# Kernel optimization log

Measured on AMD Instinct MI355X. Metric: run time of the kernel, lower is better.

## Reference

```python
import jax, jax.numpy as jnp
import numpy as np

D = 768       # feature dim (LayerNorm([768]))
NCHAR = 96    # codebook rows (char_dic = zeros(96, 768))
EPS = 1e-5    # torch LayerNorm default eps
EMA = 0.1     # EMA update coefficient


def layer_norm(x, w, b):
    mu = jnp.mean(x, axis=-1, keepdims=True)
    var = jnp.mean((x - mu) ** 2, axis=-1, keepdims=True)
    return (x - mu) * jax.lax.rsqrt(var + EPS) * w + b


def setup_inputs() -> dict:
    key = jax.random.key(0)
    k1, k2, k3 = jax.random.split(key, 3)
    B, S = 128, 1024
    return {
        "input_f": jax.random.normal(k1, (B, S, D), dtype=jnp.float32),
        "char_dic": jax.random.normal(k2, (NCHAR, D), dtype=jnp.float32),
        "ln_w": jnp.ones((D,), dtype=jnp.float32),
        "ln_b": jnp.zeros((D,), dtype=jnp.float32),
        "target": jax.random.randint(k3, (B, S), 0, NCHAR),
    }


def reference(input_f, char_dic, ln_w, ln_b, target):
    x = layer_norm(input_f, ln_w, ln_b)              # [B, S, D]
    flat = x.reshape(-1, D)                          # [N, D]
    labels = target.reshape(-1)                      # [N]
    # per-label scatter-add of token embeddings
    tok_sums = jax.ops.segment_sum(flat, labels, num_segments=NCHAR)          # [96, D]
    counts = jax.ops.segment_sum(jnp.ones_like(labels, dtype=jnp.float32),
                                 labels, num_segments=NCHAR)                  # [96]
    # group i = [char_dic[i]] + tokens with label i; row-sum of that group:
    group_sum = char_dic + tok_sums
    # sum of all pairwise dot products within a group == ||row-sum||^2
    positive = jnp.sum(group_sum * group_sum) / D
    # EMA codebook update (rows 1..95 only; row 0 untouched)
    mean = group_sum / (counts + 1.0)[:, None]       # group size = n_i + 1 (dic row)
    upd = char_dic + EMA * mean
    new_char = jnp.where(jnp.arange(NCHAR)[:, None] >= 1, upd, char_dic)
    # torch applies layer_norm1 to the updated codebook under no_grad
    normed = jax.lax.stop_gradient(layer_norm(new_char, ln_w, ln_b))
    s = jnp.sum(normed[1:], axis=0)                  # sum-of-rows identity again
    negative = jnp.dot(s, s) / D
    return negative - positive
```

## Files before the change

### kernel.cpp

```cpp
#include <hip/hip_runtime.h>

#define DD 768
#define NCH 96
#define NTOK 32
#define NBLK 128

#define WS_S1      0
#define WS_MC      294912
#define WS_GS      295296
#define WS_GPOS    298368
#define WS_CNT     298372
#define WS_ZEND    298376
#define WS_PHIST   298496
#define WS_SORTED  347648

__device__ __forceinline__ float wave_reduce_sum(float v) {
#pragma unroll
  for (int m = 32; m >= 1; m >>= 1) v += __shfl_xor(v, m, 64);
  return v;
}

__global__ void __launch_bounds__(256) k_prep(const int* __restrict__ tgt, int n, int chunk,
                                              float* __restrict__ zbase, int* __restrict__ phist) {
  __shared__ int lh[NCH];
  int tid = threadIdx.x, bid = blockIdx.x;
  if (tid < NCH) lh[tid] = 0;
  int nz = WS_ZEND / 4;
  for (int i = bid * 256 + tid; i < nz; i += NBLK * 256) zbase[i] = 0.f;
  __syncthreads();
  int beg = bid * chunk, end = min(beg + chunk, n);
  for (int i = beg + tid; i < end; i += 256) atomicAdd(&lh[tgt[i]], 1);
  __syncthreads();
  if (tid < NCH) phist[bid * NCH + tid] = lh[tid];
}

__global__ void __launch_bounds__(256) k_scatter(const int* __restrict__ tgt, int n, int chunk,
                                                 const int* __restrict__ phist,
                                                 int* __restrict__ sorted) {
  __shared__ int tot[NCH], cbase[NCH], offs_l[NCH], lcnt[NCH];
  int tid = threadIdx.x, bid = blockIdx.x;
  if (tid < NCH) {
    int s = 0, p = 0;
    for (int b = 0; b < NBLK; ++b) {
      int v = phist[b * NCH + tid];
      s += v;
      if (b < bid) p += v;
    }
    tot[tid] = s; cbase[tid] = p; lcnt[tid] = 0;
  }
  __syncthreads();
  if (tid == 0) {
    int off = 0;
    for (int c = 0; c < NCH; ++c) { offs_l[c] = off; off += tot[c]; }
  }
  __syncthreads();
  int beg = bid * chunk, end = min(beg + chunk, n);
  for (int i = beg + tid; i < end; i += 256) {
    int c = tgt[i];
    int r = atomicAdd(&lcnt[c], 1);
    sorted[offs_l[c] + cbase[c] + r] = i;
  }
}

__global__ void __launch_bounds__(256) k_main(
    const float* __restrict__ x, const int* __restrict__ sorted,
    const int* __restrict__ tgt, int n, int chunks,
    float* __restrict__ S1, float* __restrict__ Mc) {
  int w = (blockIdx.x * blockDim.x + threadIdx.x) >> 6;
  if (w >= chunks) return;
  int lane = threadIdx.x & 63;
  int beg = w * NTOK;
  int cnt = min(NTOK, n - beg);

  int tl = 0, cl = -1;
  if (lane < cnt) { tl = sorted[beg + lane]; cl = tgt[tl]; }

  int t = __shfl(tl, 0);
  int c = __shfl(cl, 0);
  const float4* r0 = (const float4*)(x + (size_t)t * DD);
  float4 A = r0[lane], B = r0[64 + lane], C = r0[128 + lane];

  float acc[12];
#pragma unroll
  for (int k = 0; k < 12; ++k) acc[k] = 0.f;
  float mcp = 0.f;

  for (int i = 0; i < cnt; ++i) {
    float4 An, Bn, Cn;
    int cn = -1;
    if (i + 1 < cnt) {
      int tn = __shfl(tl, i + 1);
      cn = __shfl(cl, i + 1);
      const float4* rn = (const float4*)(x + (size_t)tn * DD);
      An = rn[lane]; Bn = rn[64 + lane]; Cn = rn[128 + lane];
    }
    float v[12] = {A.x, A.y, A.z, A.w, B.x, B.y, B.z, B.w, C.x, C.y, C.z, C.w};
    float s = 0.f, q = 0.f;
#pragma unroll
    for (int k = 0; k < 12; ++k) { s += v[k]; q += v[k] * v[k]; }
    s = wave_reduce_sum(s);
    q = wave_reduce_sum(q);
    float mu = s * (1.f / DD);
    float var = q * (1.f / DD) - mu * mu;
    float rstd = rsqrtf(var + 1e-5f);
#pragma unroll
    for (int k = 0; k < 12; ++k) acc[k] += rstd * v[k];
    mcp += rstd * mu;

    if (cn != c) {
      float* S1r = S1 + c * DD;
#pragma unroll
      for (int k = 0; k < 12; ++k) {
        int d = (k >> 2) * 256 + 4 * lane + (k & 3);
        atomicAdd(&S1r[d], acc[k]);
      }
      if (lane == 0) atomicAdd(&Mc[c], mcp);
#pragma unroll
      for (int k = 0; k < 12; ++k) acc[k] = 0.f;
      mcp = 0.f;
      c = cn;
    }
    A = An; B = Bn; C = Cn;
  }
}

__global__ void __launch_bounds__(64) k_finish(
    const float* __restrict__ dic, const float* __restrict__ wv,
    const float* __restrict__ bv, const float* __restrict__ S1,
    const float* __restrict__ Mc, const int* __restrict__ phist,
    float* __restrict__ gS, float* __restrict__ gpos, int* __restrict__ counter,
    float* __restrict__ out) {
  int c = blockIdx.x, lane = threadIdx.x;

  float s = 0.f;
  for (int b = lane; b < NBLK; b += 64) s += (float)phist[b * NCH + c];
  float nc = wave_reduce_sum(s);

  float mc = Mc[c];
  const float* dr = dic + c * DD;
  const float* sr = S1 + c * DD;

  float g[12];
  float pacc = 0.f;
#pragma unroll
  for (int k = 0; k < 12; ++k) {
    int d = (k >> 2) * 256 + 4 * lane + (k & 3);
    float gg = dr[d] + wv[d] * (sr[d] - mc) + nc * bv[d];
    g[k] = gg;
    pacc += gg * gg;
  }
  pacc = wave_reduce_sum(pacc);
  if (lane == 0) atomicAdd(gpos, pacc);

  if (c >= 1) {
    float inv = 1.f / (nc + 1.f);
    float u[12];
    float sum = 0.f, sq = 0.f;
#pragma unroll
    for (int k = 0; k < 12; ++k) {
      int d = (k >> 2) * 256 + 4 * lane + (k & 3);
      float uu = dr[d] + 0.1f * g[k] * inv;
      u[k] = uu; sum += uu; sq += uu * uu;
    }
    sum = wave_reduce_sum(sum);
    sq = wave_reduce_sum(sq);
    float mu = sum * (1.f / DD);
    float rstd = rsqrtf(sq * (1.f / DD) - mu * mu + 1e-5f);
#pragma unroll
    for (int k = 0; k < 12; ++k) {
      int d = (k >> 2) * 256 + 4 * lane + (k & 3);
      atomicAdd(&gS[d], (u[k] - mu) * rstd * wv[d] + bv[d]);
    }
  }

  __threadfence();
  int done = 0;
  if (lane == 0) done = (atomicAdd(counter, 1) == NCH - 1) ? 1 : 0;
  done = __shfl(done, 0);
  if (done) {
    __threadfence();
    float nv = 0.f;
#pragma unroll
    for (int k = 0; k < 12; ++k) {
      int d = (k >> 2) * 256 + 4 * lane + (k & 3);
      float t = gS[d];
      nv += t * t;
    }
    nv = wave_reduce_sum(nv);
    if (lane == 0) out[0] = (nv - gpos[0]) * (1.f / DD);
  }
}

extern "C" void kernel_launch(void* const* d_in, const int* in_sizes, int n_in,
                              void* d_out, int out_size, void* d_ws, size_t ws_size,
                              hipStream_t stream) {
  (void)n_in; (void)out_size; (void)ws_size;
  const float* x   = (const float*)d_in[0];
  const float* dic = (const float*)d_in[1];
  const float* w   = (const float*)d_in[2];
  const float* b   = (const float*)d_in[3];
  const int*   tgt = (const int*)d_in[4];
  float* out = (float*)d_out;
  int N = in_sizes[4];

  char* ws = (char*)d_ws;
  float* S1     = (float*)(ws + WS_S1);
  float* Mc     = (float*)(ws + WS_MC);
  float* gS     = (float*)(ws + WS_GS);
  float* gpos   = (float*)(ws + WS_GPOS);
  int*   cnt    = (int*)(ws + WS_CNT);
  int*   phist  = (int*)(ws + WS_PHIST);
  int*   sorted = (int*)(ws + WS_SORTED);

  int chunk = (N + NBLK - 1) / NBLK;
  k_prep<<<NBLK, 256, 0, stream>>>(tgt, N, chunk, (float*)ws, phist);
  k_scatter<<<NBLK, 256, 0, stream>>>(tgt, N, chunk, phist, sorted);

  int chunks = (N + NTOK - 1) / NTOK;
  int mblocks = (chunks + 3) / 4;
  k_main<<<mblocks, 256, 0, stream>>>(x, sorted, tgt, N, chunks, S1, Mc);
  k_finish<<<NCH, 64, 0, stream>>>(dic, w, b, S1, Mc, phist, gS, gpos, cnt, out);
}
```

Before: 148.8 us.

## Replace global atomics with per-slot label-pure partial sums and block reduction

Token chunks are now aligned to label boundaries: each slot of up to 16 tokens belongs to a single class. k_main writes each slot's normalized partial row sum to a buffer with plain stores, and k_finish reduces those partials per class with four waves. This removes the scattered global float atomics on S1 and Mc, and it drops the zeroing of the large accumulator. The cost is an extra partial-sum buffer (roughly N/16 rows of 768 floats) that is written and read back, plus a fixed persistent grid of 1024 blocks for k_main.

```diff
diff --git a/kernel.cpp b/kernel.cpp
--- a/kernel.cpp
+++ b/kernel.cpp
@@ -2,17 +2,8 @@
 
 #define DD 768
 #define NCH 96
-#define NTOK 32
+#define NTOK 16
 #define NBLK 128
-
-#define WS_S1      0
-#define WS_MC      294912
-#define WS_GS      295296
-#define WS_GPOS    298368
-#define WS_CNT     298372
-#define WS_ZEND    298376
-#define WS_PHIST   298496
-#define WS_SORTED  347648
 
 __device__ __forceinline__ float wave_reduce_sum(float v) {
 #pragma unroll
@@ -25,8 +16,8 @@
   __shared__ int lh[NCH];
   int tid = threadIdx.x, bid = blockIdx.x;
   if (tid < NCH) lh[tid] = 0;
-  int nz = WS_ZEND / 4;
-  for (int i = bid * 256 + tid; i < nz; i += NBLK * 256) zbase[i] = 0.f;
+  int gi = bid * 256 + tid;
+  if (gi < 800) zbase[gi] = 0.f;
   __syncthreads();
   int beg = bid * chunk, end = min(beg + chunk, n);
   for (int i = beg + tid; i < end; i += 256) atomicAdd(&lh[tgt[i]], 1);
@@ -36,8 +27,12 @@
 
 __global__ void __launch_bounds__(256) k_scatter(const int* __restrict__ tgt, int n, int chunk,
                                                  const int* __restrict__ phist,
-                                                 int* __restrict__ sorted) {
-  __shared__ int tot[NCH], cbase[NCH], offs_l[NCH], lcnt[NCH];
+                                                 int* __restrict__ sorted,
+                                                 int* __restrict__ offs_g, int* __restrict__ sbase_g,
+                                                 int* __restrict__ nslots,
+                                                 int* __restrict__ tbase, int* __restrict__ tcnt) {
+  __shared__ int tot[NCH], cbase[NCH], lcnt[NCH];
+  __shared__ int offs_l[NCH + 1], sb_l[NCH + 1];
   int tid = threadIdx.x, bid = blockIdx.x;
   if (tid < NCH) {
     int s = 0, p = 0;
@@ -50,10 +45,26 @@
   }
   __syncthreads();
   if (tid == 0) {
-    int off = 0;
-    for (int c = 0; c < NCH; ++c) { offs_l[c] = off; off += tot[c]; }
-  }
-  __syncthreads();
+    int off = 0, sb = 0;
+    for (int c = 0; c < NCH; ++c) {
+      offs_l[c] = off; sb_l[c] = sb;
+      off += tot[c]; sb += (tot[c] + NTOK - 1) / NTOK;
+    }
+    offs_l[NCH] = off; sb_l[NCH] = sb;
+  }
+  __syncthreads();
+  if (bid == 0) {
+    for (int c = tid; c <= NCH; c += 256) { offs_g[c] = offs_l[c]; sbase_g[c] = sb_l[c]; }
+    if (tid == 0) *nslots = sb_l[NCH];
+    for (int c = tid; c < NCH; c += 256) {
+      int o = offs_l[c], ncnt = tot[c], sb = sb_l[c];
+      int nsl = (ncnt + NTOK - 1) / NTOK;
+      for (int j = 0; j < nsl; ++j) {
+        tbase[sb + j] = o + j * NTOK;
+        tcnt[sb + j] = min(NTOK, ncnt - j * NTOK);
+      }
+    }
+  }
   int beg = bid * chunk, end = min(beg + chunk, n);
   for (int i = beg + tid; i < end; i += 256) {
     int c = tgt[i];
@@ -64,130 +75,132 @@
 
 __global__ void __launch_bounds__(256) k_main(
     const float* __restrict__ x, const int* __restrict__ sorted,
-    const int* __restrict__ tgt, int n, int chunks,
-    float* __restrict__ S1, float* __restrict__ Mc) {
+    const int* __restrict__ tbase, const int* __restrict__ tcnt,
+    const int* __restrict__ nslots,
+    float* __restrict__ P, float* __restrict__ Pm) {
+  int lane = threadIdx.x & 63;
   int w = (blockIdx.x * blockDim.x + threadIdx.x) >> 6;
-  if (w >= chunks) return;
-  int lane = threadIdx.x & 63;
-  int beg = w * NTOK;
-  int cnt = min(NTOK, n - beg);
-
-  int tl = 0, cl = -1;
-  if (lane < cnt) { tl = sorted[beg + lane]; cl = tgt[tl]; }
-
-  int t = __shfl(tl, 0);
-  int c = __shfl(cl, 0);
-  const float4* r0 = (const float4*)(x + (size_t)t * DD);
-  float4 A = r0[lane], B = r0[64 + lane], C = r0[128 + lane];
-
+  int W = (gridDim.x * blockDim.x) >> 6;
+  int S = *nslots;
+  for (int s = w; s < S; s += W) {
+    int base = tbase[s], cnt = tcnt[s];
+    int tl = (lane < cnt) ? sorted[base + lane] : 0;
+    int t = __shfl(tl, 0);
+    const float4* r0 = (const float4*)(x + (size_t)t * DD);
+    float4 A = r0[lane], B = r0[64 + lane], C = r0[128 + lane];
+    float acc[12];
+#pragma unroll
+    for (int k = 0; k < 12; ++k) acc[k] = 0.f;
+    float mcp = 0.f;
+    for (int i = 0; i < cnt; ++i) {
+      float4 An, Bn, Cn;
+      if (i + 1 < cnt) {
+        int tn = __shfl(tl, i + 1);
+        const float4* rn = (const float4*)(x + (size_t)tn * DD);
+        An = rn[lane]; Bn = rn[64 + lane]; Cn = rn[128 + lane];
+      }
+      float v[12] = {A.x, A.y, A.z, A.w, B.x, B.y, B.z, B.w, C.x, C.y, C.z, C.w};
+      float ssum = 0.f, q = 0.f;
+#pragma unroll
+      for (int k = 0; k < 12; ++k) { ssum += v[k]; q += v[k] * v[k]; }
+      ssum = wave_reduce_sum(ssum);
+      q = wave_reduce_sum(q);
+      float mu = ssum * (1.f / DD);
+      float var = q * (1.f / DD) - mu * mu;
+      float rstd = rsqrtf(var + 1e-5f);
+#pragma unroll
+      for (int k = 0; k < 12; ++k) acc[k] += rstd * v[k];
+      mcp += rstd * mu;
+      A = An; B = Bn; C = Cn;
+    }
+    float4* Pr = (float4*)(P + (size_t)s * DD);
+    Pr[lane]       = make_float4(acc[0], acc[1], acc[2], acc[3]);
+    Pr[64 + lane]  = make_float4(acc[4], acc[5], acc[6], acc[7]);
+    Pr[128 + lane] = make_float4(acc[8], acc[9], acc[10], acc[11]);
+    if (lane == 0) Pm[s] = mcp;
+  }
+}
+
+__global__ void __launch_bounds__(256) k_finish(
+    const float* __restrict__ dic, const float* __restrict__ wv_,
+    const float* __restrict__ bv_, const float* __restrict__ P,
+    const float* __restrict__ Pm, const int* __restrict__ offs_g,
+    const int* __restrict__ sbase_g,
+    float* __restrict__ gS, float* __restrict__ gpos, int* __restrict__ counter,
+    float* __restrict__ out) {
+  __shared__ float accsh[DD];
+  __shared__ float mcsh;
+  int c = blockIdx.x, tid = threadIdx.x, lane = tid & 63, wid = tid >> 6;
+  for (int i = tid; i < DD; i += 256) accsh[i] = 0.f;
+  if (tid == 0) mcsh = 0.f;
+  __syncthreads();
+  int sb = sbase_g[c], se = sbase_g[c + 1];
+  float nc = (float)(offs_g[c + 1] - offs_g[c]);
   float acc[12];
 #pragma unroll
   for (int k = 0; k < 12; ++k) acc[k] = 0.f;
   float mcp = 0.f;
-
-  for (int i = 0; i < cnt; ++i) {
-    float4 An, Bn, Cn;
-    int cn = -1;
-    if (i + 1 < cnt) {
-      int tn = __shfl(tl, i + 1);
-      cn = __shfl(cl, i + 1);
-      const float4* rn = (const float4*)(x + (size_t)tn * DD);
-      An = rn[lane]; Bn = rn[64 + lane]; Cn = rn[128 + lane];
-    }
-    float v[12] = {A.x, A.y, A.z, A.w, B.x, B.y, B.z, B.w, C.x, C.y, C.z, C.w};
-    float s = 0.f, q = 0.f;
-#pragma unroll
-    for (int k = 0; k < 12; ++k) { s += v[k]; q += v[k] * v[k]; }
-    s = wave_reduce_sum(s);
-    q = wave_reduce_sum(q);
-    float mu = s * (1.f / DD);
-    float var = q * (1.f / DD) - mu * mu;
-    float rstd = rsqrtf(var + 1e-5f);
-#pragma unroll
-    for (int k = 0; k < 12; ++k) acc[k] += rstd * v[k];
-    mcp += rstd * mu;
-
-    if (cn != c) {
-      float* S1r = S1 + c * DD;
+  for (int s = sb + wid; s < se; s += 4) {
+    const float4* Pr = (const float4*)(P + (size_t)s * DD);
+    float4 A = Pr[lane], B = Pr[64 + lane], C = Pr[128 + lane];
+    acc[0] += A.x; acc[1] += A.y; acc[2]  += A.z; acc[3]  += A.w;
+    acc[4] += B.x; acc[5] += B.y; acc[6]  += B.z; acc[7]  += B.w;
+    acc[8] += C.x; acc[9] += C.y; acc[10] += C.z; acc[11] += C.w;
+    mcp += Pm[s];
+  }
+#pragma unroll
+  for (int k = 0; k < 12; ++k) {
+    int d = (k >> 2) * 256 + 4 * lane + (k & 3);
+    atomicAdd(&accsh[d], acc[k]);
+  }
+  if (lane == 0) atomicAdd(&mcsh, mcp);
+  __syncthreads();
+  if (wid == 0) {
+    float mc = mcsh;
+    float g[12], pacc = 0.f;
+#pragma unroll
+    for (int k = 0; k < 12; ++k) {
+      int d = (k >> 2) * 256 + 4 * lane + (k & 3);
+      float gg = dic[c * DD + d] + wv_[d] * (accsh[d] - mc) + nc * bv_[d];
+      g[k] = gg; pacc += gg * gg;
+    }
+    pacc = wave_reduce_sum(pacc);
+    if (lane == 0) atomicAdd(gpos, pacc);
+    if (c >= 1) {
+      float inv = 1.f / (nc + 1.f);
+      float u[12], sum = 0.f, sq = 0.f;
 #pragma unroll
       for (int k = 0; k < 12; ++k) {
         int d = (k >> 2) * 256 + 4 * lane + (k & 3);
-        atomicAdd(&S1r[d], acc[k]);
-      }
-      if (lane == 0) atomicAdd(&Mc[c], mcp);
-#pragma unroll
-      for (int k = 0; k < 12; ++k) acc[k] = 0.f;
-      mcp = 0.f;
-      c = cn;
-    }
-    A = An; B = Bn; C = Cn;
-  }
-}
-
-__global__ void __launch_bounds__(64) k_finish(
-    const float* __restrict__ dic, const float* __restrict__ wv,
-    const float* __restrict__ bv, const float* __restrict__ S1,
-    const float* __restrict__ Mc, const int* __restrict__ phist,
-    float* __restrict__ gS, float* __restrict__ gpos, int* __restrict__ counter,
-    float* __restrict__ out) {
-  int c = blockIdx.x, lane = threadIdx.x;
-
-  float s = 0.f;
-  for (int b = lane; b < NBLK; b += 64) s += (float)phist[b * NCH + c];
-  float nc = wave_reduce_sum(s);
-
-  float mc = Mc[c];
-  const float* dr = dic + c * DD;
-  const float* sr = S1 + c * DD;
-
-  float g[12];
-  float pacc = 0.f;
-#pragma unroll
-  for (int k = 0; k < 12; ++k) {
-    int d = (k >> 2) * 256 + 4 * lane + (k & 3);
-    float gg = dr[d] + wv[d] * (sr[d] - mc) + nc * bv[d];
-    g[k] = gg;
-    pacc += gg * gg;
-  }
-  pacc = wave_reduce_sum(pacc);
-  if (lane == 0) atomicAdd(gpos, pacc);
-
-  if (c >= 1) {
-    float inv = 1.f / (nc + 1.f);
-    float u[12];
-    float sum = 0.f, sq = 0.f;
-#pragma unroll
-    for (int k = 0; k < 12; ++k) {
-      int d = (k >> 2) * 256 + 4 * lane + (k & 3);
-      float uu = dr[d] + 0.1f * g[k] * inv;
-      u[k] = uu; sum += uu; sq += uu * uu;
-    }
-    sum = wave_reduce_sum(sum);
-    sq = wave_reduce_sum(sq);
-    float mu = sum * (1.f / DD);
-    float rstd = rsqrtf(sq * (1.f / DD) - mu * mu + 1e-5f);
-#pragma unroll
-    for (int k = 0; k < 12; ++k) {
-      int d = (k >> 2) * 256 + 4 * lane + (k & 3);
-      atomicAdd(&gS[d], (u[k] - mu) * rstd * wv[d] + bv[d]);
-    }
-  }
-
-  __threadfence();
-  int done = 0;
-  if (lane == 0) done = (atomicAdd(counter, 1) == NCH - 1) ? 1 : 0;
-  done = __shfl(done, 0);
-  if (done) {
+        float uu = dic[c * DD + d] + 0.1f * g[k] * inv;
+        u[k] = uu; sum += uu; sq += uu * uu;
+      }
+      sum = wave_reduce_sum(sum);
+      sq = wave_reduce_sum(sq);
+      float mu = sum * (1.f / DD);
+      float rstd = rsqrtf(sq * (1.f / DD) - mu * mu + 1e-5f);
+#pragma unroll
+      for (int k = 0; k < 12; ++k) {
+        int d = (k >> 2) * 256 + 4 * lane + (k & 3);
+        atomicAdd(&gS[d], (u[k] - mu) * rstd * wv_[d] + bv_[d]);
+      }
+    }
     __threadfence();
-    float nv = 0.f;
-#pragma unroll
-    for (int k = 0; k < 12; ++k) {
-      int d = (k >> 2) * 256 + 4 * lane + (k & 3);
-      float t = gS[d];
-      nv += t * t;
-    }
-    nv = wave_reduce_sum(nv);
-    if (lane == 0) out[0] = (nv - gpos[0]) * (1.f / DD);
+    int done = 0;
+    if (lane == 0) done = (atomicAdd(counter, 1) == NCH - 1) ? 1 : 0;
+    done = __shfl(done, 0);
+    if (done) {
+      __threadfence();
+      float nv = 0.f;
+#pragma unroll
+      for (int k = 0; k < 12; ++k) {
+        int d = (k >> 2) * 256 + 4 * lane + (k & 3);
+        float t = gS[d];
+        nv += t * t;
+      }
+      nv = wave_reduce_sum(nv);
+      if (lane == 0) out[0] = (nv - gpos[0]) * (1.f / DD);
+    }
   }
 }
 
@@ -204,20 +217,31 @@
   int N = in_sizes[4];
 
   char* ws = (char*)d_ws;
-  float* S1     = (float*)(ws + WS_S1);
-  float* Mc     = (float*)(ws + WS_MC);
-  float* gS     = (float*)(ws + WS_GS);
-  float* gpos   = (float*)(ws + WS_GPOS);
-  int*   cnt    = (int*)(ws + WS_CNT);
-  int*   phist  = (int*)(ws + WS_PHIST);
-  int*   sorted = (int*)(ws + WS_SORTED);
+  float* gS      = (float*)(ws);
+  float* gpos    = (float*)(ws + 3072);
+  int*   counter = (int*)(ws + 3076);
+  int*   offs_g  = (int*)(ws + 3200);
+  int*   sbase_g = (int*)(ws + 3648);
+  int*   nslots  = (int*)(ws + 4096);
+  int*   tbase   = (int*)(ws + 4160);
+
+  int maxslots = (N + NTOK - 1) / NTOK + NCH;
+  size_t o_tcnt = 4160 + (size_t)maxslots * 4;
+  int*   tcnt = (int*)(ws + o_tcnt);
+  size_t o_pm = o_tcnt + (size_t)maxslots * 4;
+  float* Pm = (float*)(ws + o_pm);
+  size_t o_ph = o_pm + (size_t)maxslots * 4;
+  int*   phist = (int*)(ws + o_ph);
+  size_t o_P = (o_ph + (size_t)NBLK * NCH * 4 + 255) & ~(size_t)255;
+  float* P = (float*)(ws + o_P);
+  size_t o_sorted = o_P + (size_t)maxslots * DD * 4;
+  int*   sorted = (int*)(ws + o_sorted);
 
   int chunk = (N + NBLK - 1) / NBLK;
   k_prep<<<NBLK, 256, 0, stream>>>(tgt, N, chunk, (float*)ws, phist);
-  k_scatter<<<NBLK, 256, 0, stream>>>(tgt, N, chunk, phist, sorted);
-
-  int chunks = (N + NTOK - 1) / NTOK;
-  int mblocks = (chunks + 3) / 4;
-  k_main<<<mblocks, 256, 0, stream>>>(x, sorted, tgt, N, chunks, S1, Mc);
-  k_finish<<<NCH, 64, 0, stream>>>(dic, w, b, S1, Mc, phist, gS, gpos, cnt, out);
-}
+  k_scatter<<<NBLK, 256, 0, stream>>>(tgt, N, chunk, phist, sorted,
+                                      offs_g, sbase_g, nslots, tbase, tcnt);
+  k_main<<<1024, 256, 0, stream>>>(x, sorted, tbase, tcnt, nslots, P, Pm);
+  k_finish<<<NCH, 256, 0, stream>>>(dic, w, b, P, Pm, offs_g, sbase_g,
+                                    gS, gpos, counter, out);
+}
```

Result: faster. 139.5 us (-6.3%).
